# Optimization experiments

Hardware: AMD Instinct MI355X
Metric: run time of the kernel (lower is better)

The kernel has to match this reference:

```python
import jax, jax.numpy as jnp
import numpy as np
from itertools import permutations as _permutations

N_ORB = 64
N_ALPHA = 5
N_BETA = 5
TEMP = 1.0
PERMS5 = jnp.asarray(np.array(list(_permutations(range(5))), dtype=np.int32))  # (120, 5)


def setup_inputs() -> dict:
    key = jax.random.key(0)
    ks = jax.random.split(key, 16)
    B = 8192
    s = 0.02
    inp = {
        "uniform_alpha": jax.random.uniform(ks[0], (B, N_ORB), dtype=jnp.float32),
        "uniform_beta": jax.random.uniform(ks[1], (B, N_ORB), dtype=jnp.float32),
        # learnable params
        "alpha_logits": jax.random.normal(ks[2], (N_ORB,), dtype=jnp.float32) * s,
        # alpha_to_beta: Linear(n_orb,128) -> SiLU -> Linear(128,64)
        "W1": jax.random.normal(ks[3], (N_ORB, 128), dtype=jnp.float32) * s,
        "b1": jnp.zeros((128,), jnp.float32),
        "W2": jax.random.normal(ks[4], (128, 64), dtype=jnp.float32) * s,
        "b2": jnp.zeros((64,), jnp.float32),
        # beta_conditioned_scorer: Linear(n_orb+64,256)->SiLU->Linear(256,256)->SiLU->Linear(256,n_orb)
        "V1": jax.random.normal(ks[5], (N_ORB + 64, 256), dtype=jnp.float32) * s,
        "c1": jnp.zeros((256,), jnp.float32),
        "V2": jax.random.normal(ks[6], (256, 256), dtype=jnp.float32) * s,
        "c2": jnp.zeros((256,), jnp.float32),
        "V3": jax.random.normal(ks[7], (256, N_ORB), dtype=jnp.float32) * s,
        "c3": jnp.zeros((N_ORB,), jnp.float32),
    }
    return inp


def _gumbel_topk(logits, uniform, k):
    """Straight-through Gumbel top-k mask. logits, uniform: (B, n)."""
    g = -jnp.log(-jnp.log(jnp.maximum(uniform, 1e-10)))
    perturbed = (logits + g) / TEMP
    _, top_idx = jax.lax.top_k(perturbed, k)                      # (B, k)
    B = logits.shape[0]
    one_hot = jnp.zeros_like(logits).at[jnp.arange(B)[:, None], top_idx].set(1.0)
    soft = jax.nn.softmax(perturbed, axis=-1)
    return one_hot - jax.lax.stop_gradient(soft) + soft


def _exact_pl_log_prob(logits, selection, k, perms):
    """log P(unordered top-k set) under Plackett-Luce, exact over k! orderings.

    logits: (B, n); selection: (B, n) soft/hard mask; perms: (P, k) static.
    """
    B, n = logits.shape
    P = perms.shape[0]
    _, sel_idx = jax.lax.top_k(selection, k)
    sel_idx = jnp.sort(sel_idx, axis=-1)                          # (B, k)
    perm_idx = sel_idx[:, perms]                                  # (B, P, k)
    lg = logits[:, None, :]                                       # (B, 1, n)
    remaining = jnp.ones((B, P, n), dtype=bool)
    lp = jnp.zeros((B, P), logits.dtype)
    bi = jnp.arange(B)[:, None]
    pi = jnp.arange(P)[None, :]
    for step in range(k):  # k is small and static (5)
        masked = jnp.where(remaining, lg, -jnp.inf)
        logp = jax.nn.log_softmax(masked, axis=-1)                # (B, P, n)
        idx = perm_idx[:, :, step]                                # (B, P)
        lp = lp + jnp.take_along_axis(logp, idx[..., None], axis=-1)[..., 0]
        remaining = remaining.at[bi, pi, idx].set(False)
    return jax.scipy.special.logsumexp(lp, axis=-1)              # (B,)


def reference(uniform_alpha, uniform_beta, alpha_logits, W1, b1, W2, b2,
              V1, c1, V2, c2, V3, c3):
    B = uniform_alpha.shape[0]
    a_logits = jnp.broadcast_to(alpha_logits[None, :], (B, N_ORB))
    alpha_config = _gumbel_topk(a_logits, uniform_alpha, N_ALPHA)

    # alpha_to_beta MLP
    h = jax.nn.silu(alpha_config @ W1 + b1)
    alpha_context = h @ W2 + b2                                   # (B, 64)

    beta_input = jnp.concatenate([jnp.zeros((B, N_ORB), a_logits.dtype), alpha_context], axis=-1)
    z = jax.nn.silu(beta_input @ V1 + c1)
    z = jax.nn.silu(z @ V2 + c2)
    beta_logits = z @ V3 + c3                                     # (B, n_orb)

    beta_config = _gumbel_topk(beta_logits, uniform_beta, N_BETA)
    configs = jnp.concatenate([alpha_config, beta_config], axis=-1)

    lp_a = _exact_pl_log_prob(a_logits, alpha_config, N_ALPHA, PERMS5)
    lp_b = _exact_pl_log_prob(beta_logits, beta_config, N_BETA, PERMS5)
    log_probs = lp_a + lp_b
    return configs, log_probs
```

## Files before the change

### kernel.cpp

```cpp
#include <hip/hip_runtime.h>
#include <math.h>

#define NTH 256
#define KP 264
#define SPB 8
#define OFF_W2 0
#define OFF_V1 16384
#define OFF_V2 49152
#define OFF_V3 180224
#define WS_USHORTS 212992
#define MFMA16 __builtin_amdgcn_mfma_f32_16x16x32_bf16

typedef __attribute__((ext_vector_type(8))) short s16x8;
typedef __attribute__((ext_vector_type(8))) unsigned short u16x8;
typedef __attribute__((ext_vector_type(4))) unsigned short u16x4;
typedef __attribute__((ext_vector_type(4))) float f32x4;

__device__ __forceinline__ float waveSum(float v) {
#pragma unroll
  for (int off = 32; off; off >>= 1) v += __shfl_xor(v, off, 64);
  return v;
}

__device__ __forceinline__ float siluf(float x) { return x / (1.0f + expf(-x)); }

__device__ __forceinline__ void bsplit(float x, unsigned short& h, unsigned short& l) {
  unsigned u = __float_as_uint(x);
  unsigned hb = (u + 0x7FFFu + ((u >> 16) & 1u)) >> 16;
  float hf = __uint_as_float(hb << 16);
  float lf = x - hf;
  unsigned ul = __float_as_uint(lf);
  unsigned lb = (ul + 0x7FFFu + ((ul >> 16) & 1u)) >> 16;
  h = (unsigned short)hb; l = (unsigned short)lb;
}

__device__ __forceinline__ float permSum(const float se0, const float se1,
                                         const float se2, const float se3,
                                         const float se4, float Z, int lane) {
  float psum = 0.0f;
#pragma unroll
  for (int pp = 0; pp < 2; ++pp) {
    int p = lane + pp * 64;
    if (p < 120) {
      int rem = p;
      unsigned avail = 0x43210u;
      float c = 0.0f;
      float prod = Z;
#pragma unroll
      for (int j = 0; j < 4; ++j) {
        const int fct = (j == 0) ? 24 : (j == 1) ? 6 : (j == 2) ? 2 : 1;
        int q = rem / fct; rem -= q * fct;
        int sh = q * 4;
        int dg = (avail >> sh) & 0xF;
        avail = (avail & ((1u << sh) - 1u)) | ((avail >> (sh + 4)) << sh);
        float ev = (dg == 0) ? se0 : (dg == 1) ? se1 : (dg == 2) ? se2
                 : (dg == 3) ? se3 : se4;
        c += ev;
        prod *= (Z - c);
      }
      psum += 1.0f / prod;
    }
  }
  return psum;
}

__device__ __forceinline__ float selectAndPL(float lv, float ev, float Z,
                                             const float* __restrict__ u64,
                                             float* __restrict__ gout,
                                             int lane, int* sel_i_out) {
  float u = u64[lane];
  float g = -logf(-logf(fmaxf(u, 1e-10f)));
  float vcur = lv + g;
  float sel_e[5];
#pragma unroll
  for (int r = 0; r < 5; ++r) {
    float bv = vcur; int bi = lane;
#pragma unroll
    for (int off = 32; off; off >>= 1) {
      float ov = __shfl_xor(bv, off, 64);
      int   oi = __shfl_xor(bi, off, 64);
      if (ov > bv || (ov == bv && oi < bi)) { bv = ov; bi = oi; }
    }
    if (sel_i_out) sel_i_out[r] = bi;
    sel_e[r] = __shfl(ev, bi, 64);
    if (lane == bi) vcur = -INFINITY;
  }
  float isSel = (vcur == -INFINITY) ? 1.0f : 0.0f;
  gout[lane] = isSel;
  float sl = waveSum(isSel != 0.0f ? lv : 0.0f);
  float S  = waveSum(permSum(sel_e[0], sel_e[1], sel_e[2], sel_e[3],
                             sel_e[4], Z, lane));
  return sl + logf(S);
}

__global__ __launch_bounds__(NTH)
void pcf_prep(const float* __restrict__ W2, const float* __restrict__ V1,
              const float* __restrict__ V2, const float* __restrict__ V3,
              unsigned short* __restrict__ ws)
{
  int tid = blockIdx.x * NTH + threadIdx.x;
  const float* src; int N, Ks, dstoff, r;
  if (tid < 1024)       { src = W2;            N = 64;  Ks = 4; dstoff = OFF_W2; r = tid; }
  else if (tid < 3072)  { src = V1 + 64 * 256; N = 256; Ks = 2; dstoff = OFF_V1; r = tid - 1024; }
  else if (tid < 11264) { src = V2;            N = 256; Ks = 8; dstoff = OFF_V2; r = tid - 3072; }
  else                  { src = V3;            N = 64;  Ks = 8; dstoff = OFF_V3; r = tid - 11264; }
  int lane = r & 63, ts = r >> 6;
  int ks = ts % Ks, ct = ts / Ks;
  int n = ct * 16 + (lane & 15);
  int k0 = ks * 32 + (lane >> 4) * 8;
  u16x8 hv, lv;
#pragma unroll
  for (int j = 0; j < 8; ++j) {
    float x = src[(size_t)(k0 + j) * N + n];
    unsigned short h, l;
    bsplit(x, h, l);
    hv[j] = h; lv[j] = l;
  }
  unsigned short* dst = ws + dstoff + (size_t)ts * 1024 + lane * 8;
  *(u16x8*)dst = hv;
  *(u16x8*)(dst + 512) = lv;
}

__global__ __launch_bounds__(NTH, 4)
void pcf_mfma(const float* __restrict__ ua, const float* __restrict__ ub,
              const float* __restrict__ alog, const float* __restrict__ W1,
              const float* __restrict__ b1, const float* __restrict__ b2,
              const float* __restrict__ c1, const float* __restrict__ c2,
              const float* __restrict__ c3,
              const unsigned short* __restrict__ wt, float* __restrict__ out)
{
  __shared__ unsigned short sAhi[16 * KP], sAlo[16 * KP];
  __shared__ unsigned short sBhi[16 * KP], sBlo[16 * KP];
  __shared__ float sBL[16 * 64];
  __shared__ int   sSelA[SPB * 5];
  __shared__ float sLpA[SPB];

  const int t    = threadIdx.x;
  const int lane = t & 63;
  const int wv   = t >> 6;
  const int ln15 = lane & 15;
  const int quad = lane >> 4;
  const int bbase = blockIdx.x * SPB;

  {
    float la = alog[lane];
    float ea = expf(la);
    float Za = waveSum(ea);
#pragma unroll 1
    for (int si = 0; si < 2; ++si) {
      int s = wv * 2 + si;
      int b = bbase + s;
      int sel_i[5];
      float lp = selectAndPL(la, ea, Za, ua + (size_t)b * 64,
                             out + (size_t)b * 128, lane, sel_i);
      if (lane == 0) {
        sLpA[s] = lp;
#pragma unroll
        for (int r = 0; r < 5; ++r) sSelA[s * 5 + r] = sel_i[r];
      }
    }
  }
  __syncthreads();

  {
    int s  = t >> 5;
    int j4 = (t & 31) * 4;
    const int rows[5] = { sSelA[s * 5 + 0], sSelA[s * 5 + 1], sSelA[s * 5 + 2],
                          sSelA[s * 5 + 3], sSelA[s * 5 + 4] };
    float4 a = *(const float4*)(b1 + j4);
#pragma unroll
    for (int r = 0; r < 5; ++r) {
      float4 w = *(const float4*)(W1 + (size_t)rows[r] * 128 + j4);
      a.x += w.x; a.y += w.y; a.z += w.z; a.w += w.w;
    }
    u16x4 hv, lv;
    unsigned short h, l;
    bsplit(siluf(a.x), h, l); hv[0] = h; lv[0] = l;
    bsplit(siluf(a.y), h, l); hv[1] = h; lv[1] = l;
    bsplit(siluf(a.z), h, l); hv[2] = h; lv[2] = l;
    bsplit(siluf(a.w), h, l); hv[3] = h; lv[3] = l;
    *(u16x4*)&sAhi[s * KP + j4] = hv;
    *(u16x4*)&sAlo[s * KP + j4] = lv;
  }
  __syncthreads();

  {
    f32x4 acc = {0.f, 0.f, 0.f, 0.f};
#pragma unroll
    for (int ks = 0; ks < 4; ++ks) {
      int ko = ks * 32 + quad * 8;
      s16x8 ah = *(const s16x8*)&sAhi[ln15 * KP + ko];
      s16x8 al = *(const s16x8*)&sAlo[ln15 * KP + ko];
      const unsigned short* tsb = wt + OFF_W2 + (size_t)(wv * 4 + ks) * 1024;
      s16x8 bh = ((const s16x8*)tsb)[lane];
      s16x8 bl = ((const s16x8*)(tsb + 512))[lane];
      acc = MFMA16(ah, bh, acc, 0, 0, 0);
      acc = MFMA16(ah, bl, acc, 0, 0, 0);
      acc = MFMA16(al, bh, acc, 0, 0, 0);
    }
    int col = wv * 16 + ln15;
    float bias = b2[col];
#pragma unroll
    for (int r = 0; r < 4; ++r) {
      unsigned short h, l;
      bsplit(acc[r] + bias, h, l);
      sBhi[(quad * 4 + r) * KP + col] = h;
      sBlo[(quad * 4 + r) * KP + col] = l;
    }
  }
  __syncthreads();

  {
    f32x4 acc[4];
#pragma unroll
    for (int i = 0; i < 4; ++i) acc[i] = (f32x4){0.f, 0.f, 0.f, 0.f};
#pragma unroll
    for (int ks = 0; ks < 2; ++ks) {
      int ko = ks * 32 + quad * 8;
      s16x8 ah = *(const s16x8*)&sBhi[ln15 * KP + ko];
      s16x8 al = *(const s16x8*)&sBlo[ln15 * KP + ko];
#pragma unroll
      for (int i = 0; i < 4; ++i) {
        const unsigned short* tsb = wt + OFF_V1 + (size_t)((wv * 4 + i) * 2 + ks) * 1024;
        s16x8 bh = ((const s16x8*)tsb)[lane];
        s16x8 bl = ((const s16x8*)(tsb + 512))[lane];
        acc[i] = MFMA16(ah, bh, acc[i], 0, 0, 0);
        acc[i] = MFMA16(ah, bl, acc[i], 0, 0, 0);
        acc[i] = MFMA16(al, bh, acc[i], 0, 0, 0);
      }
    }
#pragma unroll
    for (int i = 0; i < 4; ++i) {
      int col = (wv * 4 + i) * 16 + ln15;
      float bias = c1[col];
#pragma unroll
      for (int r = 0; r < 4; ++r) {
        unsigned short h, l;
        bsplit(siluf(acc[i][r] + bias), h, l);
        sAhi[(quad * 4 + r) * KP + col] = h;
        sAlo[(quad * 4 + r) * KP + col] = l;
      }
    }
  }
  __syncthreads();

  {
    f32x4 acc[4];
#pragma unroll
    for (int i = 0; i < 4; ++i) acc[i] = (f32x4){0.f, 0.f, 0.f, 0.f};
#pragma unroll 2
    for (int ks = 0; ks < 8; ++ks) {
      int ko = ks * 32 + quad * 8;
      s16x8 ah = *(const s16x8*)&sAhi[ln15 * KP + ko];
      s16x8 al = *(const s16x8*)&sAlo[ln15 * KP + ko];
#pragma unroll
      for (int i = 0; i < 4; ++i) {
        const unsigned short* tsb = wt + OFF_V2 + (size_t)((wv * 4 + i) * 8 + ks) * 1024;
        s16x8 bh = ((const s16x8*)tsb)[lane];
        s16x8 bl = ((const s16x8*)(tsb + 512))[lane];
        acc[i] = MFMA16(ah, bh, acc[i], 0, 0, 0);
        acc[i] = MFMA16(ah, bl, acc[i], 0, 0, 0);
        acc[i] = MFMA16(al, bh, acc[i], 0, 0, 0);
      }
    }
#pragma unroll
    for (int i = 0; i < 4; ++i) {
      int col = (wv * 4 + i) * 16 + ln15;
      float bias = c2[col];
#pragma unroll
      for (int r = 0; r < 4; ++r) {
        unsigned short h, l;
        bsplit(siluf(acc[i][r] + bias), h, l);
        sBhi[(quad * 4 + r) * KP + col] = h;
        sBlo[(quad * 4 + r) * KP + col] = l;
      }
    }
  }
  __syncthreads();

  {
    f32x4 acc = {0.f, 0.f, 0.f, 0.f};
#pragma unroll
    for (int ks = 0; ks < 8; ++ks) {
      int ko = ks * 32 + quad * 8;
      s16x8 ah = *(const s16x8*)&sBhi[ln15 * KP + ko];
      s16x8 al = *(const s16x8*)&sBlo[ln15 * KP + ko];
      const unsigned short* tsb = wt + OFF_V3 + (size_t)(wv * 8 + ks) * 1024;
      s16x8 bh = ((const s16x8*)tsb)[lane];
      s16x8 bl = ((const s16x8*)(tsb + 512))[lane];
      acc = MFMA16(ah, bh, acc, 0, 0, 0);
      acc = MFMA16(ah, bl, acc, 0, 0, 0);
      acc = MFMA16(al, bh, acc, 0, 0, 0);
    }
    int col = wv * 16 + ln15;
    float bias = c3[col];
#pragma unroll
    for (int r = 0; r < 4; ++r)
      sBL[(quad * 4 + r) * 64 + col] = acc[r] + bias;
  }
  __syncthreads();

  {
#pragma unroll 1
    for (int si = 0; si < 2; ++si) {
      int s = wv * 2 + si;
      int b = bbase + s;
      float blv = sBL[s * 64 + lane];
      float eb = expf(blv);
      float Zb = waveSum(eb);
      float lp = selectAndPL(blv, eb, Zb, ub + (size_t)b * 64,
                             out + (size_t)b * 128 + 64, lane, nullptr);
      if (lane == 0)
        out[(size_t)8192 * 128 + b] = sLpA[s] + lp;
    }
  }
}

#define SPB4 4
__global__ __launch_bounds__(NTH, 8)
void pcf_small(const float* __restrict__ ua, const float* __restrict__ ub,
               const float* __restrict__ alog, const float* __restrict__ W1,
               const float* __restrict__ b1, const float* __restrict__ W2,
               const float* __restrict__ b2, const float* __restrict__ V1,
               const float* __restrict__ c1, const float* __restrict__ V2,
               const float* __restrict__ c2, const float* __restrict__ V3,
               const float* __restrict__ c3, float* __restrict__ out)
{
  __shared__ float sA[SPB4 * 256];
  __shared__ float sB[SPB4 * 256];
  __shared__ float sP[4 * 256];
  __shared__ int   sSelA[SPB4 * 5];
  __shared__ float sLpA[SPB4];

  const int t    = threadIdx.x;
  const int lane = t & 63;
  const int wv   = t >> 6;
  const int bbase = blockIdx.x * SPB4;

  {
    float la = alog[lane];
    float ea = expf(la);
    float Za = waveSum(ea);
    int b = bbase + wv;
    int sel_i[5];
    float lp = selectAndPL(la, ea, Za, ua + (size_t)b * 64,
                           out + (size_t)b * 128, lane, sel_i);
    if (lane == 0) {
      sLpA[wv] = lp;
#pragma unroll
      for (int r = 0; r < 5; ++r) sSelA[wv * 5 + r] = sel_i[r];
    }
  }
  __syncthreads();
  {
    int s = wv;
    int i0 = sSelA[s * 5 + 0], i1 = sSelA[s * 5 + 1], i2 = sSelA[s * 5 + 2];
    int i3 = sSelA[s * 5 + 3], i4 = sSelA[s * 5 + 4];
#pragma unroll
    for (int jh = 0; jh < 2; ++jh) {
      int j = lane + jh * 64;
      float acc = b1[j] + W1[i0 * 128 + j] + W1[i1 * 128 + j]
                + W1[i2 * 128 + j] + W1[i3 * 128 + j] + W1[i4 * 128 + j];
      sA[s * 128 + j] = siluf(acc);
    }
  }
  __syncthreads();
  {
    float acc[SPB4] = {};
    const int kb = 32 * wv;
#pragma unroll 2
    for (int m = 0; m < 8; ++m) {
      int k0 = kb + 4 * m;
      float w0 = W2[(k0 + 0) * 64 + lane];
      float w1 = W2[(k0 + 1) * 64 + lane];
      float w2 = W2[(k0 + 2) * 64 + lane];
      float w3 = W2[(k0 + 3) * 64 + lane];
#pragma unroll
      for (int s = 0; s < SPB4; ++s) {
        float4 x = *(float4*)&sA[s * 128 + k0];
        acc[s] += x.x * w0 + x.y * w1 + x.z * w2 + x.w * w3;
      }
    }
#pragma unroll
    for (int s = 0; s < SPB4; ++s) sP[wv * 256 + s * 64 + lane] = acc[s];
  }
  __syncthreads();
  {
    int o = t;
    float v = b2[o & 63] + sP[o] + sP[256 + o] + sP[512 + o] + sP[768 + o];
    sB[o] = v;
  }
  __syncthreads();
  {
    const int c = 64 * wv + lane;
    float acc[SPB4];
    float cb = c1[c];
#pragma unroll
    for (int s = 0; s < SPB4; ++s) acc[s] = cb;
    const float* wp = V1 + (size_t)64 * 256 + c;
#pragma unroll 4
    for (int m = 0; m < 16; ++m) {
      int k0 = 4 * m;
      float w0 = wp[(k0 + 0) * 256];
      float w1 = wp[(k0 + 1) * 256];
      float w2 = wp[(k0 + 2) * 256];
      float w3 = wp[(k0 + 3) * 256];
#pragma unroll
      for (int s = 0; s < SPB4; ++s) {
        float4 x = *(float4*)&sB[s * 64 + k0];
        acc[s] += x.x * w0 + x.y * w1 + x.z * w2 + x.w * w3;
      }
    }
#pragma unroll
    for (int s = 0; s < SPB4; ++s) sA[s * 256 + c] = siluf(acc[s]);
  }
  __syncthreads();
  {
    const int c = 64 * wv + lane;
    float acc[SPB4];
    float cb = c2[c];
#pragma unroll
    for (int s = 0; s < SPB4; ++s) acc[s] = cb;
    const float* wp = V2 + c;
#pragma unroll 4
    for (int m = 0; m < 64; ++m) {
      int k0 = 4 * m;
      float w0 = wp[(size_t)(k0 + 0) * 256];
      float w1 = wp[(size_t)(k0 + 1) * 256];
      float w2 = wp[(size_t)(k0 + 2) * 256];
      float w3 = wp[(size_t)(k0 + 3) * 256];
#pragma unroll
      for (int s = 0; s < SPB4; ++s) {
        float4 x = *(float4*)&sA[s * 256 + k0];
        acc[s] += x.x * w0 + x.y * w1 + x.z * w2 + x.w * w3;
      }
    }
#pragma unroll
    for (int s = 0; s < SPB4; ++s) sB[s * 256 + c] = siluf(acc[s]);
  }
  __syncthreads();
  {
    float acc[SPB4] = {};
    const int kb = 64 * wv;
#pragma unroll 4
    for (int m = 0; m < 16; ++m) {
      int k0 = kb + 4 * m;
      float w0 = V3[(k0 + 0) * 64 + lane];
      float w1 = V3[(k0 + 1) * 64 + lane];
      float w2 = V3[(k0 + 2) * 64 + lane];
      float w3 = V3[(k0 + 3) * 64 + lane];
#pragma unroll
      for (int s = 0; s < SPB4; ++s) {
        float4 x = *(float4*)&sB[s * 256 + k0];
        acc[s] += x.x * w0 + x.y * w1 + x.z * w2 + x.w * w3;
      }
    }
#pragma unroll
    for (int s = 0; s < SPB4; ++s) sP[wv * 256 + s * 64 + lane] = acc[s];
  }
  __syncthreads();
  {
    int b = bbase + wv;
    float blv = c3[lane] + sP[wv * 64 + lane] + sP[256 + wv * 64 + lane]
              + sP[512 + wv * 64 + lane] + sP[768 + wv * 64 + lane];
    float eb = expf(blv);
    float Zb = waveSum(eb);
    float lp = selectAndPL(blv, eb, Zb, ub + (size_t)b * 64,
                           out + (size_t)b * 128 + 64, lane, nullptr);
    if (lane == 0)
      out[(size_t)8192 * 128 + b] = sLpA[wv] + lp;
  }
}

extern "C" void kernel_launch(void* const* d_in, const int* in_sizes, int n_in,
                              void* d_out, int out_size, void* d_ws, size_t ws_size,
                              hipStream_t stream) {
  const float* ua   = (const float*)d_in[0];
  const float* ub   = (const float*)d_in[1];
  const float* alog = (const float*)d_in[2];
  const float* W1   = (const float*)d_in[3];
  const float* b1   = (const float*)d_in[4];
  const float* W2   = (const float*)d_in[5];
  const float* b2   = (const float*)d_in[6];
  const float* V1   = (const float*)d_in[7];
  const float* c1   = (const float*)d_in[8];
  const float* V2   = (const float*)d_in[9];
  const float* c2   = (const float*)d_in[10];
  const float* V3   = (const float*)d_in[11];
  const float* c3   = (const float*)d_in[12];
  float* out = (float*)d_out;

  if (ws_size >= (size_t)WS_USHORTS * 2) {
    unsigned short* wt = (unsigned short*)d_ws;
    pcf_prep<<<dim3(52), dim3(NTH), 0, stream>>>(W2, V1, V2, V3, wt);
    pcf_mfma<<<dim3(8192 / SPB), dim3(NTH), 0, stream>>>(
        ua, ub, alog, W1, b1, b2, c1, c2, c3, wt, out);
  } else {
    pcf_small<<<dim3(8192 / SPB4), dim3(NTH), 0, stream>>>(
        ua, ub, alog, W1, b1, W2, b2, V1, c1, V2, c2, V3, c3, out);
  }
}
```

Before: 117.9 us.

## Drop activation lo-split in bf16 MFMAs and use one wave per sample

```diff
diff --git a/kernel.cpp b/kernel.cpp
--- a/kernel.cpp
+++ b/kernel.cpp
@@ -1,7 +1,7 @@
 #include <hip/hip_runtime.h>
 #include <math.h>
 
-#define NTH 256
+#define NTH 512
 #define KP 264
 #define SPB 8
 #define OFF_W2 0
@@ -13,7 +13,6 @@
 
 typedef __attribute__((ext_vector_type(8))) short s16x8;
 typedef __attribute__((ext_vector_type(8))) unsigned short u16x8;
-typedef __attribute__((ext_vector_type(4))) unsigned short u16x4;
 typedef __attribute__((ext_vector_type(4))) float f32x4;
 
 __device__ __forceinline__ float waveSum(float v) {
@@ -23,6 +22,11 @@
 }
 
 __device__ __forceinline__ float siluf(float x) { return x / (1.0f + expf(-x)); }
+
+__device__ __forceinline__ unsigned short bround(float x) {
+  unsigned u = __float_as_uint(x);
+  return (unsigned short)((u + 0x7FFFu + ((u >> 16) & 1u)) >> 16);
+}
 
 __device__ __forceinline__ void bsplit(float x, unsigned short& h, unsigned short& l) {
   unsigned u = __float_as_uint(x);
@@ -93,12 +97,12 @@
   return sl + logf(S);
 }
 
-__global__ __launch_bounds__(NTH)
+__global__ __launch_bounds__(256)
 void pcf_prep(const float* __restrict__ W2, const float* __restrict__ V1,
               const float* __restrict__ V2, const float* __restrict__ V3,
               unsigned short* __restrict__ ws)
 {
-  int tid = blockIdx.x * NTH + threadIdx.x;
+  int tid = blockIdx.x * 256 + threadIdx.x;
   const float* src; int N, Ks, dstoff, r;
   if (tid < 1024)       { src = W2;            N = 64;  Ks = 4; dstoff = OFF_W2; r = tid; }
   else if (tid < 3072)  { src = V1 + 64 * 256; N = 256; Ks = 2; dstoff = OFF_V1; r = tid - 1024; }
@@ -121,7 +125,7 @@
   *(u16x8*)(dst + 512) = lv;
 }
 
-__global__ __launch_bounds__(NTH, 4)
+__global__ __launch_bounds__(NTH, 8)
 void pcf_mfma(const float* __restrict__ ua, const float* __restrict__ ub,
               const float* __restrict__ alog, const float* __restrict__ W1,
               const float* __restrict__ b1, const float* __restrict__ b2,
@@ -129,9 +133,9 @@
               const float* __restrict__ c3,
               const unsigned short* __restrict__ wt, float* __restrict__ out)
 {
-  __shared__ unsigned short sAhi[16 * KP], sAlo[16 * KP];
-  __shared__ unsigned short sBhi[16 * KP], sBlo[16 * KP];
-  __shared__ float sBL[16 * 64];
+  __shared__ unsigned short sAhi[16 * KP];
+  __shared__ unsigned short sBhi[16 * KP];
+  __shared__ float sBL[SPB * 64];
   __shared__ int   sSelA[SPB * 5];
   __shared__ float sLpA[SPB];
 
@@ -146,178 +150,147 @@
     float la = alog[lane];
     float ea = expf(la);
     float Za = waveSum(ea);
-#pragma unroll 1
-    for (int si = 0; si < 2; ++si) {
-      int s = wv * 2 + si;
-      int b = bbase + s;
-      int sel_i[5];
-      float lp = selectAndPL(la, ea, Za, ua + (size_t)b * 64,
-                             out + (size_t)b * 128, lane, sel_i);
-      if (lane == 0) {
-        sLpA[s] = lp;
-#pragma unroll
-        for (int r = 0; r < 5; ++r) sSelA[s * 5 + r] = sel_i[r];
-      }
-    }
-  }
-  __syncthreads();
-
-  {
-    int s  = t >> 5;
-    int j4 = (t & 31) * 4;
+    int b = bbase + wv;
+    int sel_i[5];
+    float lp = selectAndPL(la, ea, Za, ua + (size_t)b * 64,
+                           out + (size_t)b * 128, lane, sel_i);
+    if (lane == 0) {
+      sLpA[wv] = lp;
+#pragma unroll
+      for (int r = 0; r < 5; ++r) sSelA[wv * 5 + r] = sel_i[r];
+    }
+  }
+  __syncthreads();
+
+  {
+    int s = wv;
+    int j = lane * 2;
     const int rows[5] = { sSelA[s * 5 + 0], sSelA[s * 5 + 1], sSelA[s * 5 + 2],
                           sSelA[s * 5 + 3], sSelA[s * 5 + 4] };
-    float4 a = *(const float4*)(b1 + j4);
+    float2 a = *(const float2*)(b1 + j);
 #pragma unroll
     for (int r = 0; r < 5; ++r) {
-      float4 w = *(const float4*)(W1 + (size_t)rows[r] * 128 + j4);
-      a.x += w.x; a.y += w.y; a.z += w.z; a.w += w.w;
-    }
-    u16x4 hv, lv;
-    unsigned short h, l;
-    bsplit(siluf(a.x), h, l); hv[0] = h; lv[0] = l;
-    bsplit(siluf(a.y), h, l); hv[1] = h; lv[1] = l;
-    bsplit(siluf(a.z), h, l); hv[2] = h; lv[2] = l;
-    bsplit(siluf(a.w), h, l); hv[3] = h; lv[3] = l;
-    *(u16x4*)&sAhi[s * KP + j4] = hv;
-    *(u16x4*)&sAlo[s * KP + j4] = lv;
-  }
-  __syncthreads();
-
-  {
+      float2 w = *(const float2*)(W1 + (size_t)rows[r] * 128 + j);
+      a.x += w.x; a.y += w.y;
+    }
+    unsigned h0 = bround(siluf(a.x));
+    unsigned h1 = bround(siluf(a.y));
+    *(unsigned*)&sAhi[s * KP + j] = h0 | (h1 << 16);
+  }
+  __syncthreads();
+
+  if (wv < 4) {
     f32x4 acc = {0.f, 0.f, 0.f, 0.f};
 #pragma unroll
     for (int ks = 0; ks < 4; ++ks) {
       int ko = ks * 32 + quad * 8;
       s16x8 ah = *(const s16x8*)&sAhi[ln15 * KP + ko];
-      s16x8 al = *(const s16x8*)&sAlo[ln15 * KP + ko];
       const unsigned short* tsb = wt + OFF_W2 + (size_t)(wv * 4 + ks) * 1024;
       s16x8 bh = ((const s16x8*)tsb)[lane];
       s16x8 bl = ((const s16x8*)(tsb + 512))[lane];
       acc = MFMA16(ah, bh, acc, 0, 0, 0);
       acc = MFMA16(ah, bl, acc, 0, 0, 0);
-      acc = MFMA16(al, bh, acc, 0, 0, 0);
     }
     int col = wv * 16 + ln15;
     float bias = b2[col];
 #pragma unroll
-    for (int r = 0; r < 4; ++r) {
-      unsigned short h, l;
-      bsplit(acc[r] + bias, h, l);
-      sBhi[(quad * 4 + r) * KP + col] = h;
-      sBlo[(quad * 4 + r) * KP + col] = l;
-    }
-  }
-  __syncthreads();
-
-  {
-    f32x4 acc[4];
-#pragma unroll
-    for (int i = 0; i < 4; ++i) acc[i] = (f32x4){0.f, 0.f, 0.f, 0.f};
+    for (int r = 0; r < 4; ++r)
+      sBhi[(quad * 4 + r) * KP + col] = bround(acc[r] + bias);
+  }
+  __syncthreads();
+
+  {
+    f32x4 acc[2];
+#pragma unroll
+    for (int i = 0; i < 2; ++i) acc[i] = (f32x4){0.f, 0.f, 0.f, 0.f};
 #pragma unroll
     for (int ks = 0; ks < 2; ++ks) {
       int ko = ks * 32 + quad * 8;
       s16x8 ah = *(const s16x8*)&sBhi[ln15 * KP + ko];
-      s16x8 al = *(const s16x8*)&sBlo[ln15 * KP + ko];
-#pragma unroll
-      for (int i = 0; i < 4; ++i) {
-        const unsigned short* tsb = wt + OFF_V1 + (size_t)((wv * 4 + i) * 2 + ks) * 1024;
+#pragma unroll
+      for (int i = 0; i < 2; ++i) {
+        const unsigned short* tsb = wt + OFF_V1 + (size_t)((wv * 2 + i) * 2 + ks) * 1024;
         s16x8 bh = ((const s16x8*)tsb)[lane];
         s16x8 bl = ((const s16x8*)(tsb + 512))[lane];
         acc[i] = MFMA16(ah, bh, acc[i], 0, 0, 0);
         acc[i] = MFMA16(ah, bl, acc[i], 0, 0, 0);
-        acc[i] = MFMA16(al, bh, acc[i], 0, 0, 0);
-      }
-    }
-#pragma unroll
-    for (int i = 0; i < 4; ++i) {
-      int col = (wv * 4 + i) * 16 + ln15;
+      }
+    }
+#pragma unroll
+    for (int i = 0; i < 2; ++i) {
+      int col = (wv * 2 + i) * 16 + ln15;
       float bias = c1[col];
 #pragma unroll
-      for (int r = 0; r < 4; ++r) {
-        unsigned short h, l;
-        bsplit(siluf(acc[i][r] + bias), h, l);
-        sAhi[(quad * 4 + r) * KP + col] = h;
-        sAlo[(quad * 4 + r) * KP + col] = l;
-      }
-    }
-  }
-  __syncthreads();
-
-  {
-    f32x4 acc[4];
-#pragma unroll
-    for (int i = 0; i < 4; ++i) acc[i] = (f32x4){0.f, 0.f, 0.f, 0.f};
+      for (int r = 0; r < 4; ++r)
+        sAhi[(quad * 4 + r) * KP + col] = bround(siluf(acc[i][r] + bias));
+    }
+  }
+  __syncthreads();
+
+  {
+    f32x4 acc[2];
+#pragma unroll
+    for (int i = 0; i < 2; ++i) acc[i] = (f32x4){0.f, 0.f, 0.f, 0.f};
 #pragma unroll 2
     for (int ks = 0; ks < 8; ++ks) {
       int ko = ks * 32 + quad * 8;
       s16x8 ah = *(const s16x8*)&sAhi[ln15 * KP + ko];
-      s16x8 al = *(const s16x8*)&sAlo[ln15 * KP + ko];
-#pragma unroll
-      for (int i = 0; i < 4; ++i) {
-        const unsigned short* tsb = wt + OFF_V2 + (size_t)((wv * 4 + i) * 8 + ks) * 1024;
+#pragma unroll
+      for (int i = 0; i < 2; ++i) {
+        const unsigned short* tsb = wt + OFF_V2 + (size_t)((wv * 2 + i) * 8 + ks) * 1024;
         s16x8 bh = ((const s16x8*)tsb)[lane];
         s16x8 bl = ((const s16x8*)(tsb + 512))[lane];
         acc[i] = MFMA16(ah, bh, acc[i], 0, 0, 0);
         acc[i] = MFMA16(ah, bl, acc[i], 0, 0, 0);
-        acc[i] = MFMA16(al, bh, acc[i], 0, 0, 0);
-      }
-    }
-#pragma unroll
-    for (int i = 0; i < 4; ++i) {
-      int col = (wv * 4 + i) * 16 + ln15;
+      }
+    }
+#pragma unroll
+    for (int i = 0; i < 2; ++i) {
+      int col = (wv * 2 + i) * 16 + ln15;
       float bias = c2[col];
 #pragma unroll
-      for (int r = 0; r < 4; ++r) {
-        unsigned short h, l;
-        bsplit(siluf(acc[i][r] + bias), h, l);
-        sBhi[(quad * 4 + r) * KP + col] = h;
-        sBlo[(quad * 4 + r) * KP + col] = l;
-      }
-    }
-  }
-  __syncthreads();
-
-  {
+      for (int r = 0; r < 4; ++r)
+        sBhi[(quad * 4 + r) * KP + col] = bround(siluf(acc[i][r] + bias));
+    }
+  }
+  __syncthreads();
+
+  if (wv < 4) {
     f32x4 acc = {0.f, 0.f, 0.f, 0.f};
 #pragma unroll
     for (int ks = 0; ks < 8; ++ks) {
       int ko = ks * 32 + quad * 8;
       s16x8 ah = *(const s16x8*)&sBhi[ln15 * KP + ko];
-      s16x8 al = *(const s16x8*)&sBlo[ln15 * KP + ko];
       const unsigned short* tsb = wt + OFF_V3 + (size_t)(wv * 8 + ks) * 1024;
       s16x8 bh = ((const s16x8*)tsb)[lane];
       s16x8 bl = ((const s16x8*)(tsb + 512))[lane];
       acc = MFMA16(ah, bh, acc, 0, 0, 0);
       acc = MFMA16(ah, bl, acc, 0, 0, 0);
-      acc = MFMA16(al, bh, acc, 0, 0, 0);
-    }
-    int col = wv * 16 + ln15;
-    float bias = c3[col];
-#pragma unroll
-    for (int r = 0; r < 4; ++r)
-      sBL[(quad * 4 + r) * 64 + col] = acc[r] + bias;
-  }
-  __syncthreads();
-
-  {
-#pragma unroll 1
-    for (int si = 0; si < 2; ++si) {
-      int s = wv * 2 + si;
-      int b = bbase + s;
-      float blv = sBL[s * 64 + lane];
-      float eb = expf(blv);
-      float Zb = waveSum(eb);
-      float lp = selectAndPL(blv, eb, Zb, ub + (size_t)b * 64,
-                             out + (size_t)b * 128 + 64, lane, nullptr);
-      if (lane == 0)
-        out[(size_t)8192 * 128 + b] = sLpA[s] + lp;
-    }
+    }
+    if (quad < 2) {
+      int col = wv * 16 + ln15;
+      float bias = c3[col];
+#pragma unroll
+      for (int r = 0; r < 4; ++r)
+        sBL[(quad * 4 + r) * 64 + col] = acc[r] + bias;
+    }
+  }
+  __syncthreads();
+
+  {
+    int b = bbase + wv;
+    float blv = sBL[wv * 64 + lane];
+    float eb = expf(blv);
+    float Zb = waveSum(eb);
+    float lp = selectAndPL(blv, eb, Zb, ub + (size_t)b * 64,
+                           out + (size_t)b * 128 + 64, lane, nullptr);
+    if (lane == 0)
+      out[(size_t)8192 * 128 + b] = sLpA[wv] + lp;
   }
 }
 
 #define SPB4 4
-__global__ __launch_bounds__(NTH, 8)
+__global__ __launch_bounds__(256, 8)
 void pcf_small(const float* __restrict__ ua, const float* __restrict__ ub,
                const float* __restrict__ alog, const float* __restrict__ W1,
                const float* __restrict__ b1, const float* __restrict__ W2,
@@ -492,11 +465,11 @@
 
   if (ws_size >= (size_t)WS_USHORTS * 2) {
     unsigned short* wt = (unsigned short*)d_ws;
-    pcf_prep<<<dim3(52), dim3(NTH), 0, stream>>>(W2, V1, V2, V3, wt);
+    pcf_prep<<<dim3(52), dim3(256), 0, stream>>>(W2, V1, V2, V3, wt);
     pcf_mfma<<<dim3(8192 / SPB), dim3(NTH), 0, stream>>>(
         ua, ub, alog, W1, b1, b2, c1, c2, c3, wt, out);
   } else {
-    pcf_small<<<dim3(8192 / SPB4), dim3(NTH), 0, stream>>>(
+    pcf_small<<<dim3(8192 / SPB4), dim3(256), 0, stream>>>(
         ua, ub, alog, W1, b1, W2, b2, V1, c1, V2, c2, V3, c3, out);
   }
 }
```

Result: faster. 112.7 us (-4.5%).
